# Kernel tuning notes

Hardware: AMD Instinct MI355X
Metric: run time of the kernel (lower is better)

The kernel has to match this reference:

```python
import jax, jax.numpy as jnp
import numpy as np
from jax import lax

B, N, C_IN, C_OUT = 8, 8192, 64, 128
NUM_SAMPLES, K = 2048, 32
EPS = 1e-5


def _bn(x, g, b, m, v):
    # inference-mode BatchNorm1d over channel axis 1; x: [G, C, L]
    scale = g / jnp.sqrt(v + EPS)
    return (x - m[None, :, None]) * scale[None, :, None] + b[None, :, None]


def _conv1x1(x, w):
    # kernel_size=1 Conv1d (no bias); x: [G, Cin, L], w: [Cout, Cin]
    return jnp.einsum('gck,oc->gok', x, w)


def _res_block(x, w1, g1, b1, m1, v1, w2, g2, b2, m2, v2):
    # conv-bn-relu -> conv-bn, residual add, relu (residual_factor=1.0)
    y = jax.nn.relu(_bn(_conv1x1(x, w1), g1, b1, m1, v1))
    y = _bn(_conv1x1(y, w2), g2, b2, m2, v2)
    return jax.nn.relu(y + x)


def _fps(xyz, num_samples):
    # farthest point sampling; xyz: [B,N,3] -> indices [B,S]
    b, n, _ = xyz.shape

    def step(carry, _):
        dists, last_idx = carry
        last_pt = jnp.take_along_axis(xyz, last_idx[:, None, None], axis=1)  # [B,1,3]
        d = jnp.sum((xyz - last_pt) ** 2, axis=-1)  # [B,N]
        dists = jnp.minimum(dists, d)
        nxt = jnp.argmax(dists, axis=-1).astype(jnp.int32)
        return (dists, nxt), last_idx

    init = (jnp.full((b, n), 1e10, xyz.dtype), jnp.zeros((b,), jnp.int32))
    _, idxs = lax.scan(step, init, None, length=num_samples)
    return jnp.transpose(idxs)  # [B,S]


def setup_inputs():
    key = jax.random.key(0)
    ks = jax.random.split(key, 40)
    xyz = jax.random.uniform(ks[0], (B, N, 3), jnp.float32)
    feat = jax.random.normal(ks[1], (B, N, C_IN), jnp.float32)

    def conv_w(k, o, c):
        return jax.random.normal(k, (o, c), jnp.float32) * (1.0 / np.sqrt(c).astype(np.float32))

    def bn_params(k, c):
        k1, k2, k3, k4 = jax.random.split(k, 4)
        return (1.0 + 0.1 * jax.random.normal(k1, (c,), jnp.float32),
                0.1 * jax.random.normal(k2, (c,), jnp.float32),
                0.1 * jax.random.normal(k3, (c,), jnp.float32),
                jax.random.uniform(k4, (c,), jnp.float32, 0.5, 1.5))

    inp = {'xyz': xyz, 'feat': feat}
    inp['te_w'] = conv_w(ks[2], C_OUT, 2 * C_IN)
    inp['te_g'], inp['te_b'], inp['te_m'], inp['te_v'] = bn_params(ks[3], C_OUT)
    for name, base in (('pre', 4), ('pos', 14)):
        inp[name + '_w1'] = jnp.stack([conv_w(ks[base + i], C_OUT, C_OUT) for i in range(2)])
        inp[name + '_w2'] = jnp.stack([conv_w(ks[base + 2 + i], C_OUT, C_OUT) for i in range(2)])
        bn1 = [bn_params(ks[base + 4 + i], C_OUT) for i in range(2)]
        bn2 = [bn_params(ks[base + 6 + i], C_OUT) for i in range(2)]
        for j, s in enumerate(('g', 'b', 'm', 'v')):
            inp[f'{name}_{s}1'] = jnp.stack([bn1[i][j] for i in range(2)])
            inp[f'{name}_{s}2'] = jnp.stack([bn2[i][j] for i in range(2)])
    return inp


def reference(xyz, feat, te_w, te_g, te_b, te_m, te_v,
              pre_w1, pre_w2, pre_g1, pre_b1, pre_m1, pre_v1, pre_g2, pre_b2, pre_m2, pre_v2,
              pos_w1, pos_w2, pos_g1, pos_b1, pos_m1, pos_v1, pos_g2, pos_b2, pos_m2, pos_v2):
    bsz = xyz.shape[0]
    # --- LocalGrouper: FPS centers + kNN grouping + concat center feat ---
    fps_idx = _fps(xyz, NUM_SAMPLES)                                    # [B,S]
    new_xyz = jnp.take_along_axis(xyz, fps_idx[..., None], axis=1)      # [B,S,3]
    ctr_feat = jnp.take_along_axis(feat, fps_idx[..., None], axis=1)    # [B,S,C]
    d2 = jnp.sum((new_xyz[:, :, None, :] - xyz[:, None, :, :]) ** 2, axis=-1)  # [B,S,N]
    _, knn_idx = lax.top_k(-d2, K)                                      # [B,S,K]
    grouped = feat[jnp.arange(bsz)[:, None, None], knn_idx]             # [B,S,K,C]
    ctr = jnp.broadcast_to(ctr_feat[:, :, None, :], grouped.shape)
    nf = jnp.concatenate([grouped, ctr], axis=-1)                       # [B,S,K,2C]
    # --- permute/view -> [B*S, 2C, K] ---
    x = nf.transpose(0, 1, 3, 2).reshape(bsz * NUM_SAMPLES, 2 * C_IN, K)
    x = jax.nn.relu(_bn(_conv1x1(x, te_w), te_g, te_b, te_m, te_v))     # [G,OUT,K]
    for i in range(2):
        x = _res_block(x, pre_w1[i], pre_g1[i], pre_b1[i], pre_m1[i], pre_v1[i],
                       pre_w2[i], pre_g2[i], pre_b2[i], pre_m2[i], pre_v2[i])
    x = jnp.max(x, axis=-1)                                             # adaptive_max_pool1d(.,1)
    x = x.reshape(bsz, NUM_SAMPLES, C_OUT).transpose(0, 2, 1)           # [B,OUT,S]
    for i in range(2):
        x = _res_block(x, pos_w1[i], pos_g1[i], pos_b1[i], pos_m1[i], pos_v1[i],
                       pos_w2[i], pos_g2[i], pos_b2[i], pos_m2[i], pos_v2[i])
    return new_xyz, x
```

## Files before the change

### kernel.cpp

```cpp
#include <hip/hip_runtime.h>

typedef unsigned short u16;
typedef unsigned int   u32;
typedef unsigned long long u64;

#define B_    8
#define N_    8192
#define CIN   64
#define COUT  128
#define NS    2048
#define K_    32
#define LDSPAD 136

typedef __attribute__((ext_vector_type(8))) short short8;
typedef __attribute__((ext_vector_type(4))) float f32x4;

#define MFMA16(a,b,c) __builtin_amdgcn_mfma_f32_16x16x32_bf16(a,b,c,0,0,0)

__device__ __forceinline__ u16 f2bf(float f){
  u32 u = __float_as_uint(f);
  return (u16)((u + 0x7FFFu + ((u >> 16) & 1u)) >> 16);
}
__device__ __forceinline__ float bf2f(u16 h){ u32 u = ((u32)h) << 16; return __uint_as_float(u); }
__device__ __forceinline__ u32 pack2bf(float lo, float hi){ return (u32)f2bf(lo) | ((u32)f2bf(hi) << 16); }

__global__ void wcvt_kernel(const float* __restrict__ s, u16* __restrict__ d, int n){
  int i = blockIdx.x * 256 + threadIdx.x;
  if (i < n) d[i] = f2bf(s[i]);
}

__global__ void clear_kernel(int* __restrict__ fps_idx, u32* __restrict__ done){
  int i = blockIdx.x * 256 + threadIdx.x;
  if (i < B_*NS){ fps_idx[i] = -1; done[i] = 0u; }
}

struct BnPtrs { const float* g[9]; const float* b[9]; const float* m[9]; const float* v[9]; };

__global__ void bn_pre_kernel(BnPtrs p, float* __restrict__ bns){
  int set = blockIdx.x, c = threadIdx.x;
  float sc = p.g[set][c] / sqrtf(p.v[set][c] + 1e-5f);
  bns[set*256 + c]       = sc;
  bns[set*256 + 128 + c] = p.b[set][c] - p.m[set][c] * sc;
}

struct ShFps {
  __align__(16) f32x4 PX4[4*512];
  __align__(16) f32x4 PY4[4*512];
  __align__(16) f32x4 PZ4[4*512];
  u64  kArr[2][8];
  float xA[2][8], yA[2][8], zA[2][8];
};
struct ShMid {
  __align__(16) u16 X[8][32*LDSPAD];
  __align__(16) float scr[8][128];
};
struct ShPos {
  __align__(16) u16 X[8][32*LDSPAD];
};
union ShAll { ShFps f; ShMid m; ShPos p; };

#define DPP_UMAX(x, ctrl) { \
  u32 o = (u32)__builtin_amdgcn_update_dpp((int)(x), (int)(x), ctrl, 0xf, 0xf, false); \
  x = (o > x) ? o : x; }

__device__ __forceinline__ u32 wave_umax63(u32 x){
  DPP_UMAX(x, 0x111)
  DPP_UMAX(x, 0x112)
  DPP_UMAX(x, 0x114)
  DPP_UMAX(x, 0x118)
  DPP_UMAX(x, 0x142)
  DPP_UMAX(x, 0x143)
  return (u32)__builtin_amdgcn_readlane((int)x, 63);
}

#define FPS_STEP4(j) { \
  f32x4 xv = PX4[j*512 + t]; \
  f32x4 yv = PY4[j*512 + t]; \
  f32x4 zv = PZ4[j*512 + t]; \
  FPS_ONE(j,0) FPS_ONE(j,1) FPS_ONE(j,2) FPS_ONE(j,3) }

#define FPS_ONE(j,i) { \
  float dx = xv[i] - lx; \
  float dy = yv[i] - ly; \
  float dz = zv[i] - lz; \
  float t0 = dx*dx; \
  float t1 = dy*dy; \
  float t2 = dz*dz; \
  float dd = (t0 + t1) + t2;   \
  float nd = fminf(D##j##i, dd); \
  D##j##i = nd; \
  u32 nb = __float_as_uint(nd); \
  tb##j = (nb > tb##j) ? nb : tb##j; }

#define FPS_KMIN(j,i) \
  kk = (__float_as_uint(D##j##i) == wmax && (4*j+i) < kk) ? (4*j+i) : kk;

__device__ void fps_path(const float* __restrict__ xyz, int* __restrict__ fps_idx,
                         ShFps& S, int b, int t){
  #pragma clang fp contract(off)
  const int lane = t & 63, wv = t >> 6;
  const float* xb = xyz + (size_t)b * N_ * 3;
  f32x4* PX4 = S.PX4; f32x4* PY4 = S.PY4; f32x4* PZ4 = S.PZ4;
  const int base = t * 16;
  #pragma unroll
  for (int j = 0; j < 4; ++j){
    f32x4 xv, yv, zv;
    #pragma unroll
    for (int i = 0; i < 4; ++i){
      const int p = base + 4*j + i;
      xv[i] = xb[p*3 + 0];
      yv[i] = xb[p*3 + 1];
      zv[i] = xb[p*3 + 2];
    }
    PX4[j*512 + t] = xv; PY4[j*512 + t] = yv; PZ4[j*512 + t] = zv;
  }
  if (t == 0)
    __hip_atomic_store(fps_idx + b*NS, 0, __ATOMIC_RELAXED, __HIP_MEMORY_SCOPE_AGENT);
  __syncthreads();
  float D00=1e10f,D01=1e10f,D02=1e10f,D03=1e10f;
  float D10=1e10f,D11=1e10f,D12=1e10f,D13=1e10f;
  float D20=1e10f,D21=1e10f,D22=1e10f,D23=1e10f;
  float D30=1e10f,D31=1e10f,D32=1e10f,D33=1e10f;
  const float* PXs = (const float*)PX4;
  const float* PYs = (const float*)PY4;
  const float* PZs = (const float*)PZ4;
  float lx = PXs[0], ly = PYs[0], lz = PZs[0];
  int my_pi = 0;
  for (int s = 0; s < NS - 1; ++s){
    u32 tb0 = 0, tb1 = 0, tb2 = 0, tb3 = 0;
    FPS_STEP4(0) FPS_STEP4(1) FPS_STEP4(2) FPS_STEP4(3)
    u32 ta = (tb0 > tb1) ? tb0 : tb1;
    u32 tc = (tb2 > tb3) ? tb2 : tb3;
    u32 tbm = (ta > tc) ? ta : tc;
    const u32 wmax = wave_umax63(tbm);
    const u64 mask = __ballot(tbm == wmax);
    const int fl = __ffsll((long long)mask) - 1;
    const int sl = s & 1;
    if (lane == fl){
      int kk = 64;
      FPS_KMIN(0,0) FPS_KMIN(0,1) FPS_KMIN(0,2) FPS_KMIN(0,3)
      FPS_KMIN(1,0) FPS_KMIN(1,1) FPS_KMIN(1,2) FPS_KMIN(1,3)
      FPS_KMIN(2,0) FPS_KMIN(2,1) FPS_KMIN(2,2) FPS_KMIN(2,3)
      FPS_KMIN(3,0) FPS_KMIN(3,1) FPS_KMIN(3,2) FPS_KMIN(3,3)
      const int pi = base + kk;
      S.kArr[sl][wv] = ((u64)wmax << 13) | (u64)(8191 - pi);
      const int li = ((kk >> 2)*512 + t)*4 + (kk & 3);
      S.xA[sl][wv] = PXs[li]; S.yA[sl][wv] = PYs[li]; S.zA[sl][wv] = PZs[li];
    }
    __syncthreads();
    u64 win = S.kArr[sl][0];
    float cx = S.xA[sl][0], cy = S.yA[sl][0], cz = S.zA[sl][0];
    #pragma unroll
    for (int w = 1; w < 8; ++w){
      u64 o = S.kArr[sl][w];
      float ox = S.xA[sl][w], oy = S.yA[sl][w], oz = S.zA[sl][w];
      bool c = o > win;
      win = c ? o : win; cx = c ? ox : cx; cy = c ? oy : cy; cz = c ? oz : cz;
    }
    lx = cx; ly = cy; lz = cz;
    const int pi_out = 8191 - (int)(win & 0x1FFFull);
    if (lane == (s & 7)) my_pi = pi_out;
    if ((s & 7) == 7 && t < 8)
      __hip_atomic_store(fps_idx + b*NS + s - 6 + t, my_pi,
                         __ATOMIC_RELAXED, __HIP_MEMORY_SCOPE_AGENT);
  }
  if (t < 7)
    __hip_atomic_store(fps_idx + b*NS + (NS - 7) + t, my_pi,
                       __ATOMIC_RELAXED, __HIP_MEMORY_SCOPE_AGENT);
}

__device__ __forceinline__ void zero_acc(f32x4 acc[8][2]){
  #pragma unroll
  for (int mt = 0; mt < 8; ++mt)
    #pragma unroll
    for (int nt = 0; nt < 2; ++nt){
      acc[mt][nt][0] = 0.f; acc[mt][nt][1] = 0.f; acc[mt][nt][2] = 0.f; acc[mt][nt][3] = 0.f;
    }
}

__device__ __forceinline__ void conv_step(const u16* __restrict__ W, const u16* __restrict__ Xw,
                                          int q, int l15, f32x4 acc[8][2]){
  #pragma unroll
  for (int kk = 0; kk < 4; ++kk){
    short8 b0 = *(const short8*)(Xw + l15*LDSPAD + kk*32 + q*8);
    short8 b1 = *(const short8*)(Xw + (16 + l15)*LDSPAD + kk*32 + q*8);
    #pragma unroll
    for (int mt = 0; mt < 8; ++mt){
      short8 a = *(const short8*)(W + (size_t)(mt*16 + l15)*COUT + kk*32 + q*8);
      acc[mt][0] = MFMA16(a, b0, acc[mt][0]);
      acc[mt][1] = MFMA16(a, b1, acc[mt][1]);
    }
  }
}

__device__ __forceinline__ void res_block(const u16* __restrict__ W1, const u16* __restrict__ W2,
    const float* __restrict__ bn1, const float* __restrict__ bn2,
    u16* __restrict__ Xw, int q, int l15, u32 resid[8][2][2], f32x4 acc[8][2], bool writeback){
  zero_acc(acc);
  conv_step(W1, Xw, q, l15, acc);
  #pragma unroll
  for (int mt = 0; mt < 8; ++mt){
    f32x4 sc = *(const f32x4*)(bn1 + mt*16 + q*4);
    f32x4 bi = *(const f32x4*)(bn1 + 128 + mt*16 + q*4);
    #pragma unroll
    for (int nt = 0; nt < 2; ++nt){
      float y0 = fmaxf(fmaf(acc[mt][nt][0], sc[0], bi[0]), 0.f);
      float y1 = fmaxf(fmaf(acc[mt][nt][1], sc[1], bi[1]), 0.f);
      float y2 = fmaxf(fmaf(acc[mt][nt][2], sc[2], bi[2]), 0.f);
      float y3 = fmaxf(fmaf(acc[mt][nt][3], sc[3], bi[3]), 0.f);
      *(uint2*)(Xw + (nt*16 + l15)*LDSPAD + mt*16 + q*4) = make_uint2(pack2bf(y0,y1), pack2bf(y2,y3));
    }
  }
  __syncthreads();
  zero_acc(acc);
  conv_step(W2, Xw, q, l15, acc);
  #pragma unroll
  for (int mt = 0; mt < 8; ++mt){
    f32x4 sc = *(const f32x4*)(bn2 + mt*16 + q*4);
    f32x4 bi = *(const f32x4*)(bn2 + 128 + mt*16 + q*4);
    #pragma unroll
    for (int nt = 0; nt < 2; ++nt){
      float r0 = bf2f((u16)(resid[mt][nt][0] & 0xFFFFu));
      float r1 = bf2f((u16)(resid[mt][nt][0] >> 16));
      float r2 = bf2f((u16)(resid[mt][nt][1] & 0xFFFFu));
      float r3 = bf2f((u16)(resid[mt][nt][1] >> 16));
      float y0 = fmaxf(fmaf(acc[mt][nt][0], sc[0], bi[0]) + r0, 0.f);
      float y1 = fmaxf(fmaf(acc[mt][nt][1], sc[1], bi[1]) + r1, 0.f);
      float y2 = fmaxf(fmaf(acc[mt][nt][2], sc[2], bi[2]) + r2, 0.f);
      float y3 = fmaxf(fmaf(acc[mt][nt][3], sc[3], bi[3]) + r3, 0.f);
      acc[mt][nt][0] = y0; acc[mt][nt][1] = y1; acc[mt][nt][2] = y2; acc[mt][nt][3] = y3;
      if (writeback){
        u32 p0 = pack2bf(y0,y1), p1 = pack2bf(y2,y3);
        resid[mt][nt][0] = p0; resid[mt][nt][1] = p1;
        *(uint2*)(Xw + (nt*16 + l15)*LDSPAD + mt*16 + q*4) = make_uint2(p0, p1);
      }
    }
  }
  if (writeback) __syncthreads();
}

__device__ void knnmid_path(const float* __restrict__ xyz, const float* __restrict__ feat,
    const u16* __restrict__ te_w, const u16* __restrict__ pre_w1, const u16* __restrict__ pre_w2,
    const float* __restrict__ bns, int* __restrict__ fps_idx,
    u16* __restrict__ x_mid, u32* __restrict__ done, float* __restrict__ out_xyz,
    u16* __restrict__ Xw, float* __restrict__ scrw, int g, int lane){
  #pragma clang fp contract(off)
  const int b = g >> 11;
  const float* xb = xyz + (size_t)b * N_ * 3;

  int raw;
  for (;;){
    raw = __hip_atomic_load(fps_idx + g, __ATOMIC_RELAXED, __HIP_MEMORY_SCOPE_AGENT);
    if (raw >= 0) break;
    __builtin_amdgcn_s_sleep(2);
  }
  const int ci = raw & (N_ - 1);
  const float cx = xb[ci*3], cy = xb[ci*3+1], cz = xb[ci*3+2];
  if (lane < 3) out_xyz[g*3 + lane] = xb[ci*3 + lane];

  float rd = __uint_as_float(0x7F800000u); int ri = 0x7FFFFFFF;
  float r31d = rd; int r31i = ri;
  for (int c = 0; c < N_/64; ++c){
    const int pid = c*64 + lane;
    float dx = xb[pid*3]   - cx;
    float dy = xb[pid*3+1] - cy;
    float dz = xb[pid*3+2] - cz;
    float t0 = dx*dx, t1 = dy*dy, t2 = dz*dz;
    float d2 = (t0 + t1) + t2;
    u64 m = __ballot((d2 < r31d) || (d2 == r31d && pid < r31i));
    while (m){
      int l = __ffsll((long long)m) - 1; m &= m - 1;
      float v = __shfl(d2, l); int vi = c*64 + l;
      if (!((v < r31d) || (v == r31d && vi < r31i))) continue;
      bool lt = (rd < v) || (rd == v && ri < vi);
      int pos = __popcll(__ballot(lt));
      float prd = __shfl_up(rd, 1); int pri = __shfl_up(ri, 1);
      if (lane == pos){ rd = v; ri = vi; }
      else if (lane > pos){ rd = prd; ri = pri; }
      r31d = __shfl(rd, 31); r31i = __shfl(ri, 31);
    }
  }

  const int q = lane >> 4, l15 = lane & 15;
  const float* fb = feat + (size_t)b * N_ * CIN;
  #pragma unroll
  for (int it = 0; it < 4; ++it){
    int lidx = it*64 + lane;
    int kq = lidx & 7;
    int col = it*8 + (lane >> 3);
    int nb = __shfl(ri, col) & (N_ - 1);
    f32x4 a0 = *(const f32x4*)(fb + (size_t)nb*CIN + kq*8);
    f32x4 a1 = *(const f32x4*)(fb + (size_t)nb*CIN + kq*8 + 4);
    *(uint2*)(Xw + col*LDSPAD + kq*8)     = make_uint2(pack2bf(a0[0],a0[1]), pack2bf(a0[2],a0[3]));
    *(uint2*)(Xw + col*LDSPAD + kq*8 + 4) = make_uint2(pack2bf(a1[0],a1[1]), pack2bf(a1[2],a1[3]));
    f32x4 c0 = *(const f32x4*)(fb + (size_t)ci*CIN + kq*8);
    f32x4 c1 = *(const f32x4*)(fb + (size_t)ci*CIN + kq*8 + 4);
    *(uint2*)(Xw + col*LDSPAD + 64 + kq*8)     = make_uint2(pack2bf(c0[0],c0[1]), pack2bf(c0[2],c0[3]));
    *(uint2*)(Xw + col*LDSPAD + 64 + kq*8 + 4) = make_uint2(pack2bf(c1[0],c1[1]), pack2bf(c1[2],c1[3]));
  }
  __syncthreads();

  f32x4 acc[8][2];
  u32 resid[8][2][2];
  zero_acc(acc);
  conv_step(te_w, Xw, q, l15, acc);
  #pragma unroll
  for (int mt = 0; mt < 8; ++mt){
    f32x4 sc = *(const f32x4*)(bns + mt*16 + q*4);
    f32x4 bi = *(const f32x4*)(bns + 128 + mt*16 + q*4);
    #pragma unroll
    for (int nt = 0; nt < 2; ++nt){
      float y0 = fmaxf(fmaf(acc[mt][nt][0], sc[0], bi[0]), 0.f);
      float y1 = fmaxf(fmaf(acc[mt][nt][1], sc[1], bi[1]), 0.f);
      float y2 = fmaxf(fmaf(acc[mt][nt][2], sc[2], bi[2]), 0.f);
      float y3 = fmaxf(fmaf(acc[mt][nt][3], sc[3], bi[3]), 0.f);
      u32 p0 = pack2bf(y0,y1), p1 = pack2bf(y2,y3);
      resid[mt][nt][0] = p0; resid[mt][nt][1] = p1;
      *(uint2*)(Xw + (nt*16 + l15)*LDSPAD + mt*16 + q*4) = make_uint2(p0, p1);
    }
  }
  __syncthreads();

  res_block(pre_w1,             pre_w2,             bns + 256, bns + 512,  Xw, q, l15, resid, acc, true);
  res_block(pre_w1 + COUT*COUT, pre_w2 + COUT*COUT, bns + 768, bns + 1024, Xw, q, l15, resid, acc, false);

  float mx[8][4];
  #pragma unroll
  for (int mt = 0; mt < 8; ++mt)
    #pragma unroll
    for (int r = 0; r < 4; ++r){
      float m0 = fmaxf(acc[mt][0][r], acc[mt][1][r]);
      #pragma unroll
      for (int off = 1; off < 16; off <<= 1) m0 = fmaxf(m0, __shfl_xor(m0, off));
      mx[mt][r] = m0;
    }
  if (l15 == 0){
    #pragma unroll
    for (int mt = 0; mt < 8; ++mt){
      f32x4 vv; vv[0] = mx[mt][0]; vv[1] = mx[mt][1]; vv[2] = mx[mt][2]; vv[3] = mx[mt][3];
      *(f32x4*)(scrw + mt*16 + q*4) = vv;
    }
  }
  __syncthreads();
  float v0 = scrw[lane*2], v1 = scrw[lane*2 + 1];
  *(u32*)(x_mid + (size_t)g*COUT + lane*2) = pack2bf(v0, v1);
  if (lane == 0)
    __hip_atomic_store(done + g, 1u, __ATOMIC_RELEASE, __HIP_MEMORY_SCOPE_AGENT);
}

__device__ void pos_path(const u16* __restrict__ x_mid,
    const u16* __restrict__ pos_w1, const u16* __restrict__ pos_w2,
    const float* __restrict__ bns, float* __restrict__ out_x,
    u32* __restrict__ done, u16* __restrict__ Xw, int g, int lane){
  const int q = lane >> 4, l15 = lane & 15;
  const int gc0 = g * 32;
  const int b = gc0 >> 11, s0 = gc0 & 2047;
  for (;;){
    u32 d = (lane < 32)
      ? __hip_atomic_load(done + gc0 + lane, __ATOMIC_RELAXED, __HIP_MEMORY_SCOPE_AGENT)
      : 1u;
    if (__all(d != 0)) break;
    __builtin_amdgcn_s_sleep(16);
  }
  __builtin_amdgcn_fence(__ATOMIC_ACQUIRE, "agent");
  #pragma unroll
  for (int it = 0; it < 8; ++it){
    int lidx = it*64 + lane;
    int col = lidx >> 4, kq = lidx & 15;
    uint4 v = *(const uint4*)(x_mid + (size_t)(gc0 + col)*COUT + kq*8);
    *(uint4*)(Xw + col*LDSPAD + kq*8) = v;
  }
  __syncthreads();
  u32 resid[8][2][2];
  #pragma unroll
  for (int mt = 0; mt < 8; ++mt)
    #pragma unroll
    for (int nt = 0; nt < 2; ++nt){
      uint2 rr = *(const uint2*)(Xw + (nt*16 + l15)*LDSPAD + mt*16 + q*4);
      resid[mt][nt][0] = rr.x; resid[mt][nt][1] = rr.y;
    }
  f32x4 acc[8][2];
  res_block(pos_w1,             pos_w2,             bns + 1280, bns + 1536, Xw, q, l15, resid, acc, true);
  res_block(pos_w1 + COUT*COUT, pos_w2 + COUT*COUT, bns + 1792, bns + 2048, Xw, q, l15, resid, acc, false);
  #pragma unroll
  for (int mt = 0; mt < 8; ++mt)
    #pragma unroll
    for (int nt = 0; nt < 2; ++nt)
      #pragma unroll
      for (int r = 0; r < 4; ++r){
        int row = mt*16 + q*4 + r;
        int colx = s0 + nt*16 + l15;
        out_x[(size_t)(b*COUT + row)*NS + colx] = acc[mt][nt][r];
      }
}

#define GRID_FPS    B_
#define GRID_KM     (B_*NS/8)
#define GRID_POS    (B_*NS/K_/8)

__global__ __launch_bounds__(512) void mega_kernel(
    const float* __restrict__ xyz, const float* __restrict__ feat,
    const u16* __restrict__ te_w, const u16* __restrict__ pre_w1, const u16* __restrict__ pre_w2,
    const u16* __restrict__ pos_w1, const u16* __restrict__ pos_w2,
    const float* __restrict__ bns, int* __restrict__ fps_idx,
    u16* __restrict__ x_mid, u32* __restrict__ done,
    float* __restrict__ out_xyz, float* __restrict__ out_x){
  __shared__ ShAll sh;
  const int bid = blockIdx.x;
  const int t = threadIdx.x;
  const int wid = t >> 6, lane = t & 63;
  if (bid < GRID_FPS){
    fps_path(xyz, fps_idx, sh.f, bid, t);
  } else if (bid < GRID_FPS + GRID_KM){
    const int g0 = (bid - GRID_FPS)*8;
    if (t == 0){
      while (__hip_atomic_load(fps_idx + g0 + 7, __ATOMIC_RELAXED,
                               __HIP_MEMORY_SCOPE_AGENT) < 0)
        __builtin_amdgcn_s_sleep(16);
    }
    __syncthreads();
    knnmid_path(xyz, feat, te_w, pre_w1, pre_w2, bns, fps_idx, x_mid, done, out_xyz,
                sh.m.X[wid], sh.m.scr[wid], g0 + wid, lane);
  } else {
    const int g = (bid - GRID_FPS - GRID_KM)*8 + wid;
    pos_path(x_mid, pos_w1, pos_w2, bns, out_x, done, sh.p.X[wid], g, lane);
  }
}

extern "C" void kernel_launch(void* const* d_in, const int* in_sizes, int n_in,
                              void* d_out, int out_size, void* d_ws, size_t ws_size,
                              hipStream_t stream){
  (void)in_sizes; (void)n_in; (void)out_size; (void)ws_size;
  const float* xyz    = (const float*)d_in[0];
  const float* feat   = (const float*)d_in[1];

  char* ws = (char*)d_ws;
  float* bns     = (float*)ws;
  u16*   wbf     = (u16*)(ws + 16384);
  int*   fps_idx = (int*)(ws + 16384 + 294912);
  u32*   done    = (u32*)(ws + 16384 + 294912 + 65536);
  u16*   x_mid   = (u16*)(ws + 16384 + 294912 + 65536 + 65536);
  float* out_xyz = (float*)d_out;
  float* out_x   = (float*)d_out + B_*NS*3;

  u16* te_w   = wbf;
  u16* pre_w1 = wbf + 16384;
  u16* pre_w2 = wbf + 49152;
  u16* pos_w1 = wbf + 81920;
  u16* pos_w2 = wbf + 114688;
  wcvt_kernel<<<64,  256, 0, stream>>>((const float*)d_in[2],  te_w,   16384);
  wcvt_kernel<<<128, 256, 0, stream>>>((const float*)d_in[7],  pre_w1, 32768);
  wcvt_kernel<<<128, 256, 0, stream>>>((const float*)d_in[8],  pre_w2, 32768);
  wcvt_kernel<<<128, 256, 0, stream>>>((const float*)d_in[17], pos_w1, 32768);
  wcvt_kernel<<<128, 256, 0, stream>>>((const float*)d_in[18], pos_w2, 32768);
  clear_kernel<<<64, 256, 0, stream>>>(fps_idx, done);

  BnPtrs bp;
  const int gi[9] = {3, 9, 10, 9, 10, 19, 20, 19, 20};
  const int bbi[9]= {4, 11,12, 11,12, 21, 22, 21, 22};
  const int mi[9] = {5, 13,14, 13,14, 23, 24, 23, 24};
  const int vi[9] = {6, 15,16, 15,16, 25, 26, 25, 26};
  const int of[9] = {0, 0, 0, 128,128, 0, 0, 128,128};
  for (int k = 0; k < 9; ++k){
    bp.g[k] = (const float*)d_in[gi[k]]  + of[k];
    bp.b[k] = (const float*)d_in[bbi[k]] + of[k];
    bp.m[k] = (const float*)d_in[mi[k]]  + of[k];
    bp.v[k] = (const float*)d_in[vi[k]]  + of[k];
  }

  bn_pre_kernel<<<9, 128, 0, stream>>>(bp, bns);
  mega_kernel<<<GRID_FPS + GRID_KM + GRID_POS, 512, 0, stream>>>(
      xyz, feat, te_w, pre_w1, pre_w2, pos_w1, pos_w2, bns,
      fps_idx, x_mid, done, out_xyz, out_x);
}
```

Before: 3.024 ms.

## Hold FPS point coords in registers and use packed float2 distance math

The farthest-point-sampling loop now loads each thread's 16 point coordinates from LDS into registers once, instead of re-reading them from LDS every step. It computes distances with two-wide float vectors so the compiler can emit packed FP32 ops, and tracks the max as a float. The cross-wave reduction becomes a tree of selects over one 64-bit key and one packed f32x4 coordinate per wave. Index stores are now batched every 16 steps instead of 8. This cuts LDS traffic and ALU work on the serial FPS critical path, at the cost of more VGPRs (48 coordinates plus 16 distances per thread).

```diff
diff --git a/kernel.cpp b/kernel.cpp
--- a/kernel.cpp
+++ b/kernel.cpp
@@ -14,6 +14,7 @@
 
 typedef __attribute__((ext_vector_type(8))) short short8;
 typedef __attribute__((ext_vector_type(4))) float f32x4;
+typedef __attribute__((ext_vector_type(2))) float f32x2;
 
 #define MFMA16(a,b,c) __builtin_amdgcn_mfma_f32_16x16x32_bf16(a,b,c,0,0,0)
 
@@ -47,8 +48,8 @@
   __align__(16) f32x4 PX4[4*512];
   __align__(16) f32x4 PY4[4*512];
   __align__(16) f32x4 PZ4[4*512];
-  u64  kArr[2][8];
-  float xA[2][8], yA[2][8], zA[2][8];
+  u64  keyA[2][8];
+  __align__(16) f32x4 cA[2][8];
 };
 struct ShMid {
   __align__(16) u16 X[8][32*LDSPAD];
@@ -73,27 +74,30 @@
   return (u32)__builtin_amdgcn_readlane((int)x, 63);
 }
 
-#define FPS_STEP4(j) { \
-  f32x4 xv = PX4[j*512 + t]; \
-  f32x4 yv = PY4[j*512 + t]; \
-  f32x4 zv = PZ4[j*512 + t]; \
-  FPS_ONE(j,0) FPS_ONE(j,1) FPS_ONE(j,2) FPS_ONE(j,3) }
-
-#define FPS_ONE(j,i) { \
-  float dx = xv[i] - lx; \
-  float dy = yv[i] - ly; \
-  float dz = zv[i] - lz; \
-  float t0 = dx*dx; \
-  float t1 = dy*dy; \
-  float t2 = dz*dz; \
-  float dd = (t0 + t1) + t2;   \
-  float nd = fminf(D##j##i, dd); \
-  D##j##i = nd; \
-  u32 nb = __float_as_uint(nd); \
-  tb##j = (nb > tb##j) ? nb : tb##j; }
-
-#define FPS_KMIN(j,i) \
-  kk = (__float_as_uint(D##j##i) == wmax && (4*j+i) < kk) ? (4*j+i) : kk;
+#define FPS_PAIR(m) { \
+  f32x2 dx = PXr##m - lx2; \
+  f32x2 dy = PYr##m - ly2; \
+  f32x2 dz = PZr##m - lz2; \
+  f32x2 t0 = dx*dx; \
+  f32x2 t1 = dy*dy; \
+  f32x2 t2 = dz*dz; \
+  f32x2 dd = (t0 + t1) + t2; \
+  f32x2 nd; \
+  nd.x = fminf(Dr##m.x, dd.x); \
+  nd.y = fminf(Dr##m.y, dd.y); \
+  Dr##m = nd; \
+  fmA = fmaxf(fmA, nd.x); \
+  fmB = fmaxf(fmB, nd.y); }
+
+#define FPS_KMIN2(m) { \
+  if (Dr##m.y == wmf) kk = 2*m + 1; \
+  if (Dr##m.x == wmf) kk = 2*m; }
+
+__device__ __forceinline__ void selmax(u64& ka, f32x4& ca, u64 kb, f32x4 cb){
+  bool c = kb > ka;
+  ka = c ? kb : ka;
+  ca = c ? cb : ca;
+}
 
 __device__ void fps_path(const float* __restrict__ xyz, int* __restrict__ fps_idx,
                          ShFps& S, int b, int t){
@@ -117,55 +121,64 @@
   if (t == 0)
     __hip_atomic_store(fps_idx + b*NS, 0, __ATOMIC_RELAXED, __HIP_MEMORY_SCOPE_AGENT);
   __syncthreads();
-  float D00=1e10f,D01=1e10f,D02=1e10f,D03=1e10f;
-  float D10=1e10f,D11=1e10f,D12=1e10f,D13=1e10f;
-  float D20=1e10f,D21=1e10f,D22=1e10f,D23=1e10f;
-  float D30=1e10f,D31=1e10f,D32=1e10f,D33=1e10f;
   const float* PXs = (const float*)PX4;
   const float* PYs = (const float*)PY4;
   const float* PZs = (const float*)PZ4;
-  float lx = PXs[0], ly = PYs[0], lz = PZs[0];
+  f32x2 PXr0,PXr1,PXr2,PXr3,PXr4,PXr5,PXr6,PXr7;
+  f32x2 PYr0,PYr1,PYr2,PYr3,PYr4,PYr5,PYr6,PYr7;
+  f32x2 PZr0,PZr1,PZr2,PZr3,PZr4,PZr5,PZr6,PZr7;
+  #define LOADP(jj, a, bq) { \
+    f32x4 vx = PX4[jj*512 + t]; f32x4 vy = PY4[jj*512 + t]; f32x4 vz = PZ4[jj*512 + t]; \
+    PXr##a.x = vx[0]; PXr##a.y = vx[1]; PXr##bq.x = vx[2]; PXr##bq.y = vx[3]; \
+    PYr##a.x = vy[0]; PYr##a.y = vy[1]; PYr##bq.x = vy[2]; PYr##bq.y = vy[3]; \
+    PZr##a.x = vz[0]; PZr##a.y = vz[1]; PZr##bq.x = vz[2]; PZr##bq.y = vz[3]; }
+  LOADP(0,0,1) LOADP(1,2,3) LOADP(2,4,5) LOADP(3,6,7)
+  #undef LOADP
+  f32x2 Dr0,Dr1,Dr2,Dr3,Dr4,Dr5,Dr6,Dr7;
+  Dr0=Dr1=Dr2=Dr3=Dr4=Dr5=Dr6=Dr7=(f32x2){1e10f,1e10f};
+  float sx = PXs[0], sy = PYs[0], sz = PZs[0];
+  f32x2 lx2 = {sx,sx}, ly2 = {sy,sy}, lz2 = {sz,sz};
   int my_pi = 0;
   for (int s = 0; s < NS - 1; ++s){
-    u32 tb0 = 0, tb1 = 0, tb2 = 0, tb3 = 0;
-    FPS_STEP4(0) FPS_STEP4(1) FPS_STEP4(2) FPS_STEP4(3)
-    u32 ta = (tb0 > tb1) ? tb0 : tb1;
-    u32 tc = (tb2 > tb3) ? tb2 : tb3;
-    u32 tbm = (ta > tc) ? ta : tc;
+    float fmA = 0.f, fmB = 0.f;
+    FPS_PAIR(0) FPS_PAIR(1) FPS_PAIR(2) FPS_PAIR(3)
+    FPS_PAIR(4) FPS_PAIR(5) FPS_PAIR(6) FPS_PAIR(7)
+    const float fm = fmaxf(fmA, fmB);
+    const u32 tbm = __float_as_uint(fm);
     const u32 wmax = wave_umax63(tbm);
     const u64 mask = __ballot(tbm == wmax);
     const int fl = __ffsll((long long)mask) - 1;
     const int sl = s & 1;
     if (lane == fl){
-      int kk = 64;
-      FPS_KMIN(0,0) FPS_KMIN(0,1) FPS_KMIN(0,2) FPS_KMIN(0,3)
-      FPS_KMIN(1,0) FPS_KMIN(1,1) FPS_KMIN(1,2) FPS_KMIN(1,3)
-      FPS_KMIN(2,0) FPS_KMIN(2,1) FPS_KMIN(2,2) FPS_KMIN(2,3)
-      FPS_KMIN(3,0) FPS_KMIN(3,1) FPS_KMIN(3,2) FPS_KMIN(3,3)
+      const float wmf = __uint_as_float(wmax);
+      int kk = 0;
+      FPS_KMIN2(7) FPS_KMIN2(6) FPS_KMIN2(5) FPS_KMIN2(4)
+      FPS_KMIN2(3) FPS_KMIN2(2) FPS_KMIN2(1) FPS_KMIN2(0)
       const int pi = base + kk;
-      S.kArr[sl][wv] = ((u64)wmax << 13) | (u64)(8191 - pi);
-      const int li = ((kk >> 2)*512 + t)*4 + (kk & 3);
-      S.xA[sl][wv] = PXs[li]; S.yA[sl][wv] = PYs[li]; S.zA[sl][wv] = PZs[li];
+      const int li = (kk >> 2)*2048 + t*4 + (kk & 3);
+      S.keyA[sl][wv] = ((u64)wmax << 13) | (u64)(8191 - pi);
+      f32x4 c; c[0] = PXs[li]; c[1] = PYs[li]; c[2] = PZs[li]; c[3] = 0.f;
+      S.cA[sl][wv] = c;
     }
     __syncthreads();
-    u64 win = S.kArr[sl][0];
-    float cx = S.xA[sl][0], cy = S.yA[sl][0], cz = S.zA[sl][0];
-    #pragma unroll
-    for (int w = 1; w < 8; ++w){
-      u64 o = S.kArr[sl][w];
-      float ox = S.xA[sl][w], oy = S.yA[sl][w], oz = S.zA[sl][w];
-      bool c = o > win;
-      win = c ? o : win; cx = c ? ox : cx; cy = c ? oy : cy; cz = c ? oz : cz;
-    }
-    lx = cx; ly = cy; lz = cz;
-    const int pi_out = 8191 - (int)(win & 0x1FFFull);
-    if (lane == (s & 7)) my_pi = pi_out;
-    if ((s & 7) == 7 && t < 8)
-      __hip_atomic_store(fps_idx + b*NS + s - 6 + t, my_pi,
+    u64 k0 = S.keyA[sl][0], k1 = S.keyA[sl][1], k2 = S.keyA[sl][2], k3 = S.keyA[sl][3];
+    u64 k4 = S.keyA[sl][4], k5 = S.keyA[sl][5], k6 = S.keyA[sl][6], k7 = S.keyA[sl][7];
+    f32x4 c0 = S.cA[sl][0], c1 = S.cA[sl][1], c2 = S.cA[sl][2], c3 = S.cA[sl][3];
+    f32x4 c4 = S.cA[sl][4], c5 = S.cA[sl][5], c6 = S.cA[sl][6], c7 = S.cA[sl][7];
+    selmax(k0,c0,k1,c1); selmax(k2,c2,k3,c3); selmax(k4,c4,k5,c5); selmax(k6,c6,k7,c7);
+    selmax(k0,c0,k2,c2); selmax(k4,c4,k6,c6);
+    selmax(k0,c0,k4,c4);
+    lx2.x = c0[0]; lx2.y = c0[0];
+    ly2.x = c0[1]; ly2.y = c0[1];
+    lz2.x = c0[2]; lz2.y = c0[2];
+    const int pi_out = 8191 - (int)(k0 & 0x1FFFull);
+    if (lane == (s & 15)) my_pi = pi_out;
+    if ((s & 15) == 15 && t < 16)
+      __hip_atomic_store(fps_idx + b*NS + s - 14 + t, my_pi,
                          __ATOMIC_RELAXED, __HIP_MEMORY_SCOPE_AGENT);
   }
-  if (t < 7)
-    __hip_atomic_store(fps_idx + b*NS + (NS - 7) + t, my_pi,
+  if (t < 15)
+    __hip_atomic_store(fps_idx + b*NS + (NS - 15) + t, my_pi,
                        __ATOMIC_RELAXED, __HIP_MEMORY_SCOPE_AGENT);
 }
 
```

After: 3.029 ms. About the same (+0.2%).
